# Performance work log

Hardware: AMD Instinct MI355X
Metric: run time of the kernel (lower is better)

Reference implementation:

```python
import jax, jax.numpy as jnp
import numpy as np

NUM_LAYERS = 2
VOCAB = 32000
IN_FEAT = 256          # embedding dim is IN_FEAT-1, +1 for cue scalar
HIDDEN = 256
ATN = 64               # hardcoded atn_feature_size in GraphConvolution
CLASSES = 2
B, N = 8, 2048


def setup_inputs() -> dict:
    key = jax.random.key(0)
    ks = jax.random.split(key, 12)
    x = jax.random.randint(ks[0], (B, N), 0, VOCAB, dtype=jnp.int32)
    cue = jax.random.randint(ks[1], (B, N), 0, 2, dtype=jnp.int32)
    adj = (jax.random.uniform(ks[2], (B, N, N)) < 0.01).astype(jnp.float32)
    s = 1.0 / np.sqrt(HIDDEN)
    emb_table = jax.random.normal(ks[3], (VOCAB, IN_FEAT - 1), jnp.float32) * 0.02
    Wh = jax.random.uniform(ks[4], (IN_FEAT, HIDDEN), jnp.float32, -s, s)
    bh = jax.random.uniform(ks[5], (HIDDEN,), jnp.float32, -s, s)
    Wq = jax.random.uniform(ks[6], (HIDDEN, ATN), jnp.float32, -s, s)
    Wk = jax.random.uniform(ks[7], (HIDDEN, ATN), jnp.float32, -s, s)
    Wv = jax.random.uniform(ks[8], (HIDDEN, HIDDEN), jnp.float32, -s, s)
    gcb = jax.random.uniform(ks[9], (HIDDEN,), jnp.float32, -s, s)
    Wc = jax.random.uniform(ks[10], (HIDDEN, CLASSES), jnp.float32, -s, s)
    bc = jax.random.uniform(ks[11], (CLASSES,), jnp.float32, -s, s)
    return {"x": x, "cue": cue, "adj": adj, "emb_table": emb_table,
            "Wh": Wh, "bh": bh, "Wq": Wq, "Wk": Wk, "Wv": Wv,
            "gcb": gcb, "Wc": Wc, "bc": bc}


def graph_attention_layer(h, adj, Wq, Wk, Wv, gcb):
    # h: [B,N,H]; adj: [B,N,N] binary. Per node i: softmax over neighbors j of
    # (Wk h_j) . (Wq h_i), weighted sum of Wv h_j. Zero-degree nodes get 0 (pre-bias).
    q = jnp.einsum('bnh,ha->bna', h, Wq)        # [B,N,A]
    k = jnp.einsum('bnh,ha->bna', h, Wk)        # [B,N,A]
    v = jnp.einsum('bnh,hg->bng', h, Wv)        # [B,N,H]
    logits = jnp.einsum('bia,bja->bij', q, k)   # [B,N,N]
    mask = adj > 0
    attn = jax.nn.softmax(jnp.where(mask, logits, -1e9), axis=-1)
    out = jnp.einsum('bij,bjh->bih', attn, v)   # [B,N,H]
    has_nbr = jnp.any(mask, axis=-1, keepdims=True)  # [B,N,1]
    return jnp.where(has_nbr, out, 0.0) + gcb


def reference(x, cue, adj, emb_table, Wh, bh, Wq, Wk, Wv, gcb, Wc, bc):
    emb = emb_table[x]                                   # [B,N,IN_FEAT-1]
    feats = jnp.concatenate([emb, cue.astype(jnp.float32)[..., None]], axis=-1)
    h = jax.nn.relu(jnp.einsum('bnf,fh->bnh', feats, Wh) + bh)
    for _ in range(NUM_LAYERS):
        h = jax.nn.sigmoid(graph_attention_layer(h, adj, Wq, Wk, Wv, gcb))
    logits = jnp.einsum('bnh,hc->bnc', h, Wc) + bc
    return jax.nn.softmax(logits, axis=-1)
```

## Files before the change

kernel.cpp:

```cpp
#include <hip/hip_runtime.h>
#include <hip/hip_bf16.h>


#define NB 8
#define NN 2048
#define ROWS (NB * NN)
#define MAXD 64
#define CSR1 6144

typedef float f4 __attribute__((ext_vector_type(4)));
typedef _Float16 hf;
typedef _Float16 hx2 __attribute__((ext_vector_type(2)));
typedef _Float16 hx4 __attribute__((ext_vector_type(4)));
typedef _Float16 hx8 __attribute__((ext_vector_type(8)));
typedef unsigned int u32;
typedef unsigned short u16;
typedef u16 us8 __attribute__((ext_vector_type(8)));

__device__ __forceinline__ float sigmoidf_(float x) { return 1.f / (1.f + __expf(-x)); }
__device__ __forceinline__ hx2 u2h(u32 u) { union { u32 u; hx2 h; } c; c.u = u; return c.h; }
__device__ __forceinline__ float dot2_(hx2 a, hx2 b, float c) {
#if __has_builtin(__builtin_amdgcn_fdot2)
    return __builtin_amdgcn_fdot2(a, b, c, false);
#else
    return c + (float)a.x * (float)b.x + (float)a.y * (float)b.y;
#endif
}
__device__ __forceinline__ u32 permlo_(u32 hi, u32 lo) { return __builtin_amdgcn_perm(hi, lo, 0x05040100u); }
__device__ __forceinline__ u32 permhi_(u32 hi, u32 lo) { return __builtin_amdgcn_perm(hi, lo, 0x07060302u); }

__device__ __forceinline__ void csr_row(const float* __restrict__ adj,
                                        int* __restrict__ deg, int* __restrict__ nbr,
                                        int row, int t, int* cnt) {
    const f4* ar4 = (const f4*)(adj + (size_t)row * NN);
    if (t == 0) *cnt = 0;
    __syncthreads();
    int* nr = nbr + (size_t)row * MAXD;
#pragma unroll
    for (int it = 0; it < 2; ++it) {
        int idx = it * 256 + t;
        f4 vv = __builtin_nontemporal_load(ar4 + idx);
        if (vv.x > 0.f) { int p = atomicAdd(cnt, 1); if (p < MAXD) nr[p] = idx * 4 + 0; }
        if (vv.y > 0.f) { int p = atomicAdd(cnt, 1); if (p < MAXD) nr[p] = idx * 4 + 1; }
        if (vv.z > 0.f) { int p = atomicAdd(cnt, 1); if (p < MAXD) nr[p] = idx * 4 + 2; }
        if (vv.w > 0.f) { int p = atomicAdd(cnt, 1); if (p < MAXD) nr[p] = idx * 4 + 3; }
    }
    __syncthreads();
    if (t == 0) deg[row] = (*cnt < MAXD) ? *cnt : MAXD;
}

__global__ __launch_bounds__(256) void k_front1(
        const int* __restrict__ x, const int* __restrict__ cue,
        const float* __restrict__ adj, const float* __restrict__ emb,
        const float* __restrict__ Wh, const float* __restrict__ bh,
        const float* __restrict__ Wq, const float* __restrict__ Wk,
        const float* __restrict__ Wv,
        hf* __restrict__ hB, hf* __restrict__ Wpt,
        int* __restrict__ deg, int* __restrict__ nbr) {
    __shared__ float As[32 * 64];
    __shared__ float Ws[32 * 128];
    int bid = blockIdx.x;
    int t = threadIdx.x;

    if (bid < 512) {
        int row0 = (bid >> 1) * 64, col0 = (bid & 1) * 128;
        int srow = t & 63, skg = t >> 6;
        int swc = (t & 31) * 4, swk = t >> 5;
        int tx = t & 15, ty = t >> 4;
        int xr = x[row0 + srow];
        float cv = (float)cue[row0 + srow];
        const float* er = emb + (size_t)xr * 255;

        float acc[4][8];
#pragma unroll
        for (int i = 0; i < 4; ++i)
#pragma unroll
            for (int j = 0; j < 8; ++j) acc[i][j] = 0.f;

        for (int kc = 0; kc < 256; kc += 32) {
            int kb = skg * 8;
#pragma unroll
            for (int u = 0; u < 8; ++u) {
                int f = kc + kb + u;
                As[(kb + u) * 64 + srow] = (f < 255) ? er[f] : cv;
            }
#pragma unroll
            for (int r = 0; r < 4; ++r) {
                int kk = swk + r * 8;
                f4 w = *(const f4*)(Wh + (size_t)(kc + kk) * 256 + col0 + swc);
                *(f4*)&Ws[kk * 128 + swc] = w;
            }
            __syncthreads();
#pragma unroll
            for (int k = 0; k < 32; ++k) {
                f4 av = *(f4*)&As[k * 64 + ty * 4];
                f4 w0 = *(f4*)&Ws[k * 128 + tx * 8];
                f4 w1 = *(f4*)&Ws[k * 128 + tx * 8 + 4];
                float a[4] = {av.x, av.y, av.z, av.w};
                float w[8] = {w0.x, w0.y, w0.z, w0.w, w1.x, w1.y, w1.z, w1.w};
#pragma unroll
                for (int i = 0; i < 4; ++i)
#pragma unroll
                    for (int j = 0; j < 8; ++j) acc[i][j] += a[i] * w[j];
            }
            __syncthreads();
        }
        f4 b0 = *(const f4*)(bh + col0 + tx * 8);
        f4 b1 = *(const f4*)(bh + col0 + tx * 8 + 4);
        float bb[8] = {b0.x, b0.y, b0.z, b0.w, b1.x, b1.y, b1.z, b1.w};
#pragma unroll
        for (int i = 0; i < 4; ++i) {
            int row = row0 + ty * 4 + i;
            hx8 o;
#pragma unroll
            for (int j = 0; j < 8; ++j) o[j] = (hf)fmaxf(acc[i][j] + bb[j], 0.f);
            *(hx8*)(hB + (size_t)row * 256 + col0 + tx * 8) = o;
        }
        return;
    }

    if (bid < 608) {
        int base = (bid - 512) * 256 + t;
#pragma unroll
        for (int r = 0; r < 4; ++r) {
            int i = base + r * 96 * 256;
            int c = i >> 8, f = i & 255;
            float v;
            if (c < 64)       v = Wq[f * 64 + c];
            else if (c < 128) v = Wk[f * 64 + (c - 64)];
            else              v = Wv[f * 256 + (c - 128)];
            Wpt[i] = (hf)v;
        }
        return;
    }

    csr_row(adj, deg, nbr, bid - 608, t, (int*)As);
}

union QSMem {
    struct { u16 As[64 * 40]; u16 Bs[128 * 40]; } q;
    int cnt;
};

__device__ __forceinline__ void qkv_tile(const hf* __restrict__ hB,
                                         const hf* __restrict__ Wpt,
                                         hf* __restrict__ qkvB,
                                         int tile, int t, QSMem& sm) {
    int col0 = (tile % 3) * 128, row0 = (tile / 3) * 64;
    int wave = t >> 6, lane = t & 63;
    int l16 = lane & 15, quad = lane >> 4;
    f4 acc[4][2];
#pragma unroll
    for (int i = 0; i < 4; ++i) { acc[i][0] = (f4){0,0,0,0}; acc[i][1] = (f4){0,0,0,0}; }
    int ar = t >> 2, ao = (t & 3) * 8;
    int bcs = t >> 1, bo = (t & 1) * 16;
    const u16* hB16 = (const u16*)hB;
    const u16* Wp16 = (const u16*)Wpt;

    for (int kc = 0; kc < 256; kc += 32) {
        us8 av  = *(const us8*)(hB16 + (size_t)(row0 + ar) * 256 + kc + ao);
        us8 bv0 = *(const us8*)(Wp16 + (size_t)(col0 + bcs) * 256 + kc + bo);
        us8 bv1 = *(const us8*)(Wp16 + (size_t)(col0 + bcs) * 256 + kc + bo + 8);
        __syncthreads();
        *(us8*)&sm.q.As[ar * 40 + ao] = av;
        *(us8*)&sm.q.Bs[bcs * 40 + bo] = bv0;
        *(us8*)&sm.q.Bs[bcs * 40 + bo + 8] = bv1;
        __syncthreads();
        hx8 afr[4], bfr[2];
#pragma unroll
        for (int mt = 0; mt < 4; ++mt)
            afr[mt] = *(hx8*)&sm.q.As[(mt * 16 + l16) * 40 + quad * 8];
#pragma unroll
        for (int nt = 0; nt < 2; ++nt)
            bfr[nt] = *(hx8*)&sm.q.Bs[((wave * 2 + nt) * 16 + l16) * 40 + quad * 8];
#pragma unroll
        for (int mt = 0; mt < 4; ++mt)
#pragma unroll
            for (int nt = 0; nt < 2; ++nt)
                acc[mt][nt] = __builtin_amdgcn_mfma_f32_16x16x32_f16(
                    afr[mt], bfr[nt], acc[mt][nt], 0, 0, 0);
    }
#pragma unroll
    for (int mt = 0; mt < 4; ++mt)
#pragma unroll
        for (int nt = 0; nt < 2; ++nt) {
            int c = col0 + (wave * 2 + nt) * 16 + l16;
#pragma unroll
            for (int reg = 0; reg < 4; ++reg) {
                int r = row0 + mt * 16 + quad * 4 + reg;
                qkvB[(size_t)r * 384 + c] = (hf)acc[mt][nt][reg];
            }
        }
}

__global__ __launch_bounds__(256) void k_qkv_csr(const hf* __restrict__ hB,
                                                 const hf* __restrict__ Wpt,
                                                 hf* __restrict__ qkvB,
                                                 const float* __restrict__ adj,
                                                 int* __restrict__ deg,
                                                 int* __restrict__ nbr) {
    __shared__ QSMem sm;
    int bid = blockIdx.x, t = threadIdx.x;
    if (bid < 768) qkv_tile(hB, Wpt, qkvB, bid, t, sm);
    else           csr_row(adj, deg, nbr, CSR1 + (bid - 768), t, &sm.cnt);
}

__global__ __launch_bounds__(256) void k_qkv(const hf* __restrict__ hB,
                                             const hf* __restrict__ Wpt,
                                             hf* __restrict__ qkvB) {
    __shared__ QSMem sm;
    qkv_tile(hB, Wpt, qkvB, blockIdx.x, threadIdx.x, sm);
}

template <bool WRITE_OUT>
__global__ __launch_bounds__(256) void k_attn(const hf* __restrict__ qkvB,
                                              const int* __restrict__ deg,
                                              const int* __restrict__ nbr,
                                              const float* __restrict__ gcb,
                                              const float* __restrict__ Wc,
                                              const float* __restrict__ bc,
                                              hf* __restrict__ hB,
                                              float* __restrict__ out) {
    int wave = threadIdx.x >> 6;
    int lane = threadIdx.x & 63;
    int bid = blockIdx.x;
    int row = (bid & 7) * NN + (bid >> 3) * 4 + wave;
    int d = deg[row];
    f4 g4 = *(const f4*)(gcb + lane * 4);
    float h0, h1, h2c, h3;
    if (d == 0) {
        h0 = sigmoidf_(g4.x); h1 = sigmoidf_(g4.y);
        h2c = sigmoidf_(g4.z); h3 = sigmoidf_(g4.w);
    } else {
        const int* jl = nbr + (size_t)row * MAXD;
        int bbase = row & ~(NN - 1);
        int jlane = jl[lane < d ? lane : 0];
        int sub = lane & 3;

        const uint4* qp = (const uint4*)(qkvB + (size_t)row * 384 + sub * 16);
        uint4 qa = qp[0], qb = qp[1];
        float pp[4] = {-1e30f, -1e30f, -1e30f, -1e30f};
#pragma unroll
        for (int pi = 0; pi < 4; ++pi) {
            if (pi * 16 < d) {
                int e = pi * 16 + (lane >> 2);
                int j = __shfl(jlane, e < d ? e : 0);
                float p = -1e30f;
                if (e < d) {
                    const uint4* kp = (const uint4*)(qkvB + (size_t)(bbase + j) * 384 + 64 + sub * 16);
                    uint4 ka = kp[0], kb = kp[1];
                    p = dot2_(u2h(ka.x), u2h(qa.x),
                        dot2_(u2h(ka.y), u2h(qa.y),
                        dot2_(u2h(ka.z), u2h(qa.z),
                        dot2_(u2h(ka.w), u2h(qa.w),
                        dot2_(u2h(kb.x), u2h(qb.x),
                        dot2_(u2h(kb.y), u2h(qb.y),
                        dot2_(u2h(kb.z), u2h(qb.z),
                        dot2_(u2h(kb.w), u2h(qb.w), 0.f))))))));
                }
                p += __shfl_xor(p, 1);
                p += __shfl_xor(p, 2);
                pp[pi] = p;
            }
        }
        int src = (lane & 15) << 2;
        float t0 = __shfl(pp[0], src), t1 = __shfl(pp[1], src);
        float t2 = __shfl(pp[2], src), t3 = __shfl(pp[3], src);
        int hi = lane >> 4;
        float pe = hi == 0 ? t0 : hi == 1 ? t1 : hi == 2 ? t2 : t3;
        if (lane >= d) pe = -1e30f;

        float mx = pe;
#pragma unroll
        for (int off = 32; off; off >>= 1) mx = fmaxf(mx, __shfl_xor(mx, off));
        float wv = __expf(pe - mx);
        float sv = wv;
#pragma unroll
        for (int off = 32; off; off >>= 1) sv += __shfl_xor(sv, off);
        float wn = wv * (1.f / sv);

        f4 a = {0, 0, 0, 0};
        for (int g = 0; g < d; g += 4) {
            float w0 = __shfl(wn, g),     w1 = __shfl(wn, g + 1);
            float w2 = __shfl(wn, g + 2), w3 = __shfl(wn, g + 3);
            int j0 = __shfl(jlane, g),     j1 = __shfl(jlane, g + 1);
            int j2 = __shfl(jlane, g + 2), j3 = __shfl(jlane, g + 3);
            hx2 w01, w23;
            w01.x = (hf)w0; w01.y = (hf)w1;
            w23.x = (hf)w2; w23.y = (hf)w3;
            uint2 v0 = *(const uint2*)(qkvB + (size_t)(bbase + j0) * 384 + 128 + lane * 4);
            uint2 v1 = *(const uint2*)(qkvB + (size_t)(bbase + j1) * 384 + 128 + lane * 4);
            uint2 v2 = *(const uint2*)(qkvB + (size_t)(bbase + j2) * 384 + 128 + lane * 4);
            uint2 v3 = *(const uint2*)(qkvB + (size_t)(bbase + j3) * 384 + 128 + lane * 4);
            a.x = dot2_(u2h(permlo_(v1.x, v0.x)), w01,
                  dot2_(u2h(permlo_(v3.x, v2.x)), w23, a.x));
            a.y = dot2_(u2h(permhi_(v1.x, v0.x)), w01,
                  dot2_(u2h(permhi_(v3.x, v2.x)), w23, a.y));
            a.z = dot2_(u2h(permlo_(v1.y, v0.y)), w01,
                  dot2_(u2h(permlo_(v3.y, v2.y)), w23, a.z));
            a.w = dot2_(u2h(permhi_(v1.y, v0.y)), w01,
                  dot2_(u2h(permhi_(v3.y, v2.y)), w23, a.w));
        }
        h0 = sigmoidf_(a.x + g4.x);
        h1 = sigmoidf_(a.y + g4.y);
        h2c = sigmoidf_(a.z + g4.z);
        h3 = sigmoidf_(a.w + g4.w);
    }
    if (!WRITE_OUT) {
        hx4 o; o.x = (hf)h0; o.y = (hf)h1; o.z = (hf)h2c; o.w = (hf)h3;
        *(hx4*)(hB + (size_t)row * 256 + lane * 4) = o;
    } else {
        f4 wc0 = *(const f4*)(Wc + lane * 8);
        f4 wc1 = *(const f4*)(Wc + lane * 8 + 4);
        float pa = h0 * wc0.x + h1 * wc0.z + h2c * wc1.x + h3 * wc1.z;
        float pb = h0 * wc0.y + h1 * wc0.w + h2c * wc1.y + h3 * wc1.w;
#pragma unroll
        for (int off = 32; off; off >>= 1) {
            pa += __shfl_xor(pa, off);
            pb += __shfl_xor(pb, off);
        }
        if (lane == 0) {
            float l0 = pa + bc[0], l1 = pb + bc[1];
            float m2 = fmaxf(l0, l1);
            float e0 = __expf(l0 - m2), e1 = __expf(l1 - m2);
            float inv2 = 1.f / (e0 + e1);
            out[(size_t)row * 2 + 0] = e0 * inv2;
            out[(size_t)row * 2 + 1] = e1 * inv2;
        }
    }
}

extern "C" void kernel_launch(void* const* d_in, const int* in_sizes, int n_in,
                              void* d_out, int out_size, void* d_ws, size_t ws_size,
                              hipStream_t stream) {
    const int*   x    = (const int*)d_in[0];
    const int*   cue  = (const int*)d_in[1];
    const float* adj  = (const float*)d_in[2];
    const float* emb  = (const float*)d_in[3];
    const float* Wh   = (const float*)d_in[4];
    const float* bh   = (const float*)d_in[5];
    const float* Wq   = (const float*)d_in[6];
    const float* Wk   = (const float*)d_in[7];
    const float* Wv   = (const float*)d_in[8];
    const float* gcb  = (const float*)d_in[9];
    const float* Wc   = (const float*)d_in[10];
    const float* bc   = (const float*)d_in[11];
    float* out = (float*)d_out;

    char* w = (char*)d_ws;
    hf*  hB   = (hf*)w;   w += (size_t)ROWS * 256 * 2;
    hf*  qkvB = (hf*)w;   w += (size_t)ROWS * 384 * 2;
    hf*  Wpt  = (hf*)w;   w += (size_t)384 * 256 * 2;
    int* deg  = (int*)w;  w += (size_t)ROWS * 4;
    int* nbr  = (int*)w;

    k_front1<<<608 + CSR1, 256, 0, stream>>>(
        x, cue, adj, emb, Wh, bh, Wq, Wk, Wv, hB, Wpt, deg, nbr);
    k_qkv_csr<<<768 + (ROWS - CSR1), 256, 0, stream>>>(hB, Wpt, qkvB, adj, deg, nbr);
    k_attn<false><<<ROWS / 4, 256, 0, stream>>>(qkvB, deg, nbr, gcb, Wc, bc, hB, out);
    k_qkv<<<768, 256, 0, stream>>>(hB, Wpt, qkvB);
    k_attn<true><<<ROWS / 4, 256, 0, stream>>>(qkvB, deg, nbr, gcb, Wc, bc, hB, out);
}
```

Baseline: 342.2 us.

## Merge all stages into one persistent kernel with grid barriers and dynamic CSR queue

Replaces the five separate launches with a single persistent 1024-block kernel whose phases (embedding GEMM plus weight packing, CSR construction, QKV GEMM, attention, repeated for the second layer) are separated by atomic-counter grid barriers. CSR rows are handed out through a global work counter so blocks that finish the embedding early take more of the adjacency scan. The goal is to remove launch gaps and tail effects between kernels. In exchange it depends on all 1024 blocks being co-resident, since the spin barrier can otherwise hang or time out, and each barrier adds spin overhead and fences.

```diff
diff --git a/kernel.cpp b/kernel.cpp
--- a/kernel.cpp
+++ b/kernel.cpp
@@ -6,7 +6,8 @@
 #define NN 2048
 #define ROWS (NB * NN)
 #define MAXD 64
-#define CSR1 6144
+#define GRID 1024
+#define TPB 256
 
 typedef float f4 __attribute__((ext_vector_type(4)));
 typedef _Float16 hf;
@@ -29,13 +30,114 @@
 __device__ __forceinline__ u32 permlo_(u32 hi, u32 lo) { return __builtin_amdgcn_perm(hi, lo, 0x05040100u); }
 __device__ __forceinline__ u32 permhi_(u32 hi, u32 lo) { return __builtin_amdgcn_perm(hi, lo, 0x07060302u); }
 
-__device__ __forceinline__ void csr_row(const float* __restrict__ adj,
-                                        int* __restrict__ deg, int* __restrict__ nbr,
-                                        int row, int t, int* cnt) {
-    const f4* ar4 = (const f4*)(adj + (size_t)row * NN);
+struct Args {
+    const int *x, *cue;
+    const float *adj, *emb, *Wh, *bh, *Wq, *Wk, *Wv, *gcb, *Wc, *bc;
+    hf *hB, *qkvB, *Wpt;
+    int *deg, *nbr;
+    int *ctrl;
+    float *out;
+};
+
+union SBig {
+    struct { float As[32 * 64]; float Ws[32 * 128]; } e;
+    struct { u16 As[64 * 40]; u16 Bs[128 * 40]; } q;
+};
+struct SCtl { int srow; int cnt; };
+
+__device__ __forceinline__ void gsync(int* bar, int target) {
+    __syncthreads();
+    if (threadIdx.x == 0) {
+        __threadfence();
+        atomicAdd(bar, 1);
+        int guard = 0;
+        while (__hip_atomic_load(bar, __ATOMIC_RELAXED, __HIP_MEMORY_SCOPE_AGENT) < target
+               && ++guard < (1 << 25))
+            __builtin_amdgcn_s_sleep(2);
+        __threadfence();
+    }
+    __syncthreads();
+}
+
+__global__ __launch_bounds__(64) void k_init(int* ctrl) {
+    if (threadIdx.x < 2) ctrl[threadIdx.x] = 0;
+}
+
+__device__ __forceinline__ void pack_w(const Args& A, int pb, int t) {
+    int base = pb * 256 + t;
+#pragma unroll
+    for (int r = 0; r < 4; ++r) {
+        int i = base + r * 96 * 256;
+        int c = i >> 8, f = i & 255;
+        float v;
+        if (c < 64)       v = A.Wq[f * 64 + c];
+        else if (c < 128) v = A.Wk[f * 64 + (c - 64)];
+        else              v = A.Wv[f * 256 + (c - 128)];
+        A.Wpt[i] = (hf)v;
+    }
+}
+
+__device__ void embed_tile(const Args& A, int tile, int t, SBig& sb) {
+    int row0 = (tile >> 1) * 64, col0 = (tile & 1) * 128;
+    int srow = t & 63, skg = t >> 6;
+    int swc = (t & 31) * 4, swk = t >> 5;
+    int tx = t & 15, ty = t >> 4;
+    int xr = A.x[row0 + srow];
+    float cv = (float)A.cue[row0 + srow];
+    const float* er = A.emb + (size_t)xr * 255;
+
+    float acc[4][8];
+#pragma unroll
+    for (int i = 0; i < 4; ++i)
+#pragma unroll
+        for (int j = 0; j < 8; ++j) acc[i][j] = 0.f;
+
+    for (int kc = 0; kc < 256; kc += 32) {
+        int kb = skg * 8;
+#pragma unroll
+        for (int u = 0; u < 8; ++u) {
+            int f = kc + kb + u;
+            sb.e.As[(kb + u) * 64 + srow] = (f < 255) ? er[f] : cv;
+        }
+#pragma unroll
+        for (int r = 0; r < 4; ++r) {
+            int kk = swk + r * 8;
+            f4 w = *(const f4*)(A.Wh + (size_t)(kc + kk) * 256 + col0 + swc);
+            *(f4*)&sb.e.Ws[kk * 128 + swc] = w;
+        }
+        __syncthreads();
+#pragma unroll
+        for (int k = 0; k < 32; ++k) {
+            f4 av = *(f4*)&sb.e.As[k * 64 + ty * 4];
+            f4 w0 = *(f4*)&sb.e.Ws[k * 128 + tx * 8];
+            f4 w1 = *(f4*)&sb.e.Ws[k * 128 + tx * 8 + 4];
+            float a[4] = {av.x, av.y, av.z, av.w};
+            float w[8] = {w0.x, w0.y, w0.z, w0.w, w1.x, w1.y, w1.z, w1.w};
+#pragma unroll
+            for (int i = 0; i < 4; ++i)
+#pragma unroll
+                for (int j = 0; j < 8; ++j) acc[i][j] += a[i] * w[j];
+        }
+        __syncthreads();
+    }
+    f4 b0 = *(const f4*)(A.bh + col0 + tx * 8);
+    f4 b1 = *(const f4*)(A.bh + col0 + tx * 8 + 4);
+    float bb[8] = {b0.x, b0.y, b0.z, b0.w, b1.x, b1.y, b1.z, b1.w};
+#pragma unroll
+    for (int i = 0; i < 4; ++i) {
+        int row = row0 + ty * 4 + i;
+        hx8 o;
+#pragma unroll
+        for (int j = 0; j < 8; ++j) o[j] = (hf)fmaxf(acc[i][j] + bb[j], 0.f);
+        *(hx8*)(A.hB + (size_t)row * 256 + col0 + tx * 8) = o;
+    }
+}
+
+__device__ __forceinline__ void csr_row(const Args& A, int row, int t, int* cnt) {
+    const f4* ar4 = (const f4*)(A.adj + (size_t)row * NN);
     if (t == 0) *cnt = 0;
     __syncthreads();
-    int* nr = nbr + (size_t)row * MAXD;
+    int* nr = A.nbr + (size_t)row * MAXD;
 #pragma unroll
     for (int it = 0; it < 2; ++it) {
         int idx = it * 256 + t;
@@ -46,106 +148,10 @@
         if (vv.w > 0.f) { int p = atomicAdd(cnt, 1); if (p < MAXD) nr[p] = idx * 4 + 3; }
     }
     __syncthreads();
-    if (t == 0) deg[row] = (*cnt < MAXD) ? *cnt : MAXD;
-}
-
-__global__ __launch_bounds__(256) void k_front1(
-        const int* __restrict__ x, const int* __restrict__ cue,
-        const float* __restrict__ adj, const float* __restrict__ emb,
-        const float* __restrict__ Wh, const float* __restrict__ bh,
-        const float* __restrict__ Wq, const float* __restrict__ Wk,
-        const float* __restrict__ Wv,
-        hf* __restrict__ hB, hf* __restrict__ Wpt,
-        int* __restrict__ deg, int* __restrict__ nbr) {
-    __shared__ float As[32 * 64];
-    __shared__ float Ws[32 * 128];
-    int bid = blockIdx.x;
-    int t = threadIdx.x;
-
-    if (bid < 512) {
-        int row0 = (bid >> 1) * 64, col0 = (bid & 1) * 128;
-        int srow = t & 63, skg = t >> 6;
-        int swc = (t & 31) * 4, swk = t >> 5;
-        int tx = t & 15, ty = t >> 4;
-        int xr = x[row0 + srow];
-        float cv = (float)cue[row0 + srow];
-        const float* er = emb + (size_t)xr * 255;
-
-        float acc[4][8];
-#pragma unroll
-        for (int i = 0; i < 4; ++i)
-#pragma unroll
-            for (int j = 0; j < 8; ++j) acc[i][j] = 0.f;
-
-        for (int kc = 0; kc < 256; kc += 32) {
-            int kb = skg * 8;
-#pragma unroll
-            for (int u = 0; u < 8; ++u) {
-                int f = kc + kb + u;
-                As[(kb + u) * 64 + srow] = (f < 255) ? er[f] : cv;
-            }
-#pragma unroll
-            for (int r = 0; r < 4; ++r) {
-                int kk = swk + r * 8;
-                f4 w = *(const f4*)(Wh + (size_t)(kc + kk) * 256 + col0 + swc);
-                *(f4*)&Ws[kk * 128 + swc] = w;
-            }
-            __syncthreads();
-#pragma unroll
-            for (int k = 0; k < 32; ++k) {
-                f4 av = *(f4*)&As[k * 64 + ty * 4];
-                f4 w0 = *(f4*)&Ws[k * 128 + tx * 8];
-                f4 w1 = *(f4*)&Ws[k * 128 + tx * 8 + 4];
-                float a[4] = {av.x, av.y, av.z, av.w};
-                float w[8] = {w0.x, w0.y, w0.z, w0.w, w1.x, w1.y, w1.z, w1.w};
-#pragma unroll
-                for (int i = 0; i < 4; ++i)
-#pragma unroll
-                    for (int j = 0; j < 8; ++j) acc[i][j] += a[i] * w[j];
-            }
-            __syncthreads();
-        }
-        f4 b0 = *(const f4*)(bh + col0 + tx * 8);
-        f4 b1 = *(const f4*)(bh + col0 + tx * 8 + 4);
-        float bb[8] = {b0.x, b0.y, b0.z, b0.w, b1.x, b1.y, b1.z, b1.w};
-#pragma unroll
-        for (int i = 0; i < 4; ++i) {
-            int row = row0 + ty * 4 + i;
-            hx8 o;
-#pragma unroll
-            for (int j = 0; j < 8; ++j) o[j] = (hf)fmaxf(acc[i][j] + bb[j], 0.f);
-            *(hx8*)(hB + (size_t)row * 256 + col0 + tx * 8) = o;
-        }
-        return;
-    }
-
-    if (bid < 608) {
-        int base = (bid - 512) * 256 + t;
-#pragma unroll
-        for (int r = 0; r < 4; ++r) {
-            int i = base + r * 96 * 256;
-            int c = i >> 8, f = i & 255;
-            float v;
-            if (c < 64)       v = Wq[f * 64 + c];
-            else if (c < 128) v = Wk[f * 64 + (c - 64)];
-            else              v = Wv[f * 256 + (c - 128)];
-            Wpt[i] = (hf)v;
-        }
-        return;
-    }
-
-    csr_row(adj, deg, nbr, bid - 608, t, (int*)As);
-}
-
-union QSMem {
-    struct { u16 As[64 * 40]; u16 Bs[128 * 40]; } q;
-    int cnt;
-};
-
-__device__ __forceinline__ void qkv_tile(const hf* __restrict__ hB,
-                                         const hf* __restrict__ Wpt,
-                                         hf* __restrict__ qkvB,
-                                         int tile, int t, QSMem& sm) {
+    if (t == 0) A.deg[row] = (*cnt < MAXD) ? *cnt : MAXD;
+}
+
+__device__ void qkv_tile(const Args& A, int tile, int t, SBig& sb) {
     int col0 = (tile % 3) * 128, row0 = (tile / 3) * 64;
     int wave = t >> 6, lane = t & 63;
     int l16 = lane & 15, quad = lane >> 4;
@@ -154,25 +160,25 @@
     for (int i = 0; i < 4; ++i) { acc[i][0] = (f4){0,0,0,0}; acc[i][1] = (f4){0,0,0,0}; }
     int ar = t >> 2, ao = (t & 3) * 8;
     int bcs = t >> 1, bo = (t & 1) * 16;
-    const u16* hB16 = (const u16*)hB;
-    const u16* Wp16 = (const u16*)Wpt;
+    const u16* hB16 = (const u16*)A.hB;
+    const u16* Wp16 = (const u16*)A.Wpt;
 
     for (int kc = 0; kc < 256; kc += 32) {
         us8 av  = *(const us8*)(hB16 + (size_t)(row0 + ar) * 256 + kc + ao);
         us8 bv0 = *(const us8*)(Wp16 + (size_t)(col0 + bcs) * 256 + kc + bo);
         us8 bv1 = *(const us8*)(Wp16 + (size_t)(col0 + bcs) * 256 + kc + bo + 8);
         __syncthreads();
-        *(us8*)&sm.q.As[ar * 40 + ao] = av;
-        *(us8*)&sm.q.Bs[bcs * 40 + bo] = bv0;
-        *(us8*)&sm.q.Bs[bcs * 40 + bo + 8] = bv1;
+        *(us8*)&sb.q.As[ar * 40 + ao] = av;
+        *(us8*)&sb.q.Bs[bcs * 40 + bo] = bv0;
+        *(us8*)&sb.q.Bs[bcs * 40 + bo + 8] = bv1;
         __syncthreads();
         hx8 afr[4], bfr[2];
 #pragma unroll
         for (int mt = 0; mt < 4; ++mt)
-            afr[mt] = *(hx8*)&sm.q.As[(mt * 16 + l16) * 40 + quad * 8];
+            afr[mt] = *(hx8*)&sb.q.As[(mt * 16 + l16) * 40 + quad * 8];
 #pragma unroll
         for (int nt = 0; nt < 2; ++nt)
-            bfr[nt] = *(hx8*)&sm.q.Bs[((wave * 2 + nt) * 16 + l16) * 40 + quad * 8];
+            bfr[nt] = *(hx8*)&sb.q.Bs[((wave * 2 + nt) * 16 + l16) * 40 + quad * 8];
 #pragma unroll
         for (int mt = 0; mt < 4; ++mt)
 #pragma unroll
@@ -188,51 +194,21 @@
 #pragma unroll
             for (int reg = 0; reg < 4; ++reg) {
                 int r = row0 + mt * 16 + quad * 4 + reg;
-                qkvB[(size_t)r * 384 + c] = (hf)acc[mt][nt][reg];
+                A.qkvB[(size_t)r * 384 + c] = (hf)acc[mt][nt][reg];
             }
         }
 }
 
-__global__ __launch_bounds__(256) void k_qkv_csr(const hf* __restrict__ hB,
-                                                 const hf* __restrict__ Wpt,
-                                                 hf* __restrict__ qkvB,
-                                                 const float* __restrict__ adj,
-                                                 int* __restrict__ deg,
-                                                 int* __restrict__ nbr) {
-    __shared__ QSMem sm;
-    int bid = blockIdx.x, t = threadIdx.x;
-    if (bid < 768) qkv_tile(hB, Wpt, qkvB, bid, t, sm);
-    else           csr_row(adj, deg, nbr, CSR1 + (bid - 768), t, &sm.cnt);
-}
-
-__global__ __launch_bounds__(256) void k_qkv(const hf* __restrict__ hB,
-                                             const hf* __restrict__ Wpt,
-                                             hf* __restrict__ qkvB) {
-    __shared__ QSMem sm;
-    qkv_tile(hB, Wpt, qkvB, blockIdx.x, threadIdx.x, sm);
-}
-
-template <bool WRITE_OUT>
-__global__ __launch_bounds__(256) void k_attn(const hf* __restrict__ qkvB,
-                                              const int* __restrict__ deg,
-                                              const int* __restrict__ nbr,
-                                              const float* __restrict__ gcb,
-                                              const float* __restrict__ Wc,
-                                              const float* __restrict__ bc,
-                                              hf* __restrict__ hB,
-                                              float* __restrict__ out) {
-    int wave = threadIdx.x >> 6;
-    int lane = threadIdx.x & 63;
-    int bid = blockIdx.x;
-    int row = (bid & 7) * NN + (bid >> 3) * 4 + wave;
-    int d = deg[row];
-    f4 g4 = *(const f4*)(gcb + lane * 4);
+__device__ void attn_row(const Args& A, int row, int lane, bool write_out) {
+    int d = A.deg[row];
+    f4 g4 = *(const f4*)(A.gcb + lane * 4);
     float h0, h1, h2c, h3;
     if (d == 0) {
         h0 = sigmoidf_(g4.x); h1 = sigmoidf_(g4.y);
         h2c = sigmoidf_(g4.z); h3 = sigmoidf_(g4.w);
     } else {
-        const int* jl = nbr + (size_t)row * MAXD;
+        const hf* qkvB = A.qkvB;
+        const int* jl = A.nbr + (size_t)row * MAXD;
         int bbase = row & ~(NN - 1);
         int jlane = jl[lane < d ? lane : 0];
         int sub = lane & 3;
@@ -306,12 +282,12 @@
         h2c = sigmoidf_(a.z + g4.z);
         h3 = sigmoidf_(a.w + g4.w);
     }
-    if (!WRITE_OUT) {
+    if (!write_out) {
         hx4 o; o.x = (hf)h0; o.y = (hf)h1; o.z = (hf)h2c; o.w = (hf)h3;
-        *(hx4*)(hB + (size_t)row * 256 + lane * 4) = o;
+        *(hx4*)(A.hB + (size_t)row * 256 + lane * 4) = o;
     } else {
-        f4 wc0 = *(const f4*)(Wc + lane * 8);
-        f4 wc1 = *(const f4*)(Wc + lane * 8 + 4);
+        f4 wc0 = *(const f4*)(A.Wc + lane * 8);
+        f4 wc1 = *(const f4*)(A.Wc + lane * 8 + 4);
         float pa = h0 * wc0.x + h1 * wc0.z + h2c * wc1.x + h3 * wc1.z;
         float pb = h0 * wc0.y + h1 * wc0.w + h2c * wc1.y + h3 * wc1.w;
 #pragma unroll
@@ -320,44 +296,76 @@
             pb += __shfl_xor(pb, off);
         }
         if (lane == 0) {
-            float l0 = pa + bc[0], l1 = pb + bc[1];
+            float l0 = pa + A.bc[0], l1 = pb + A.bc[1];
             float m2 = fmaxf(l0, l1);
             float e0 = __expf(l0 - m2), e1 = __expf(l1 - m2);
             float inv2 = 1.f / (e0 + e1);
-            out[(size_t)row * 2 + 0] = e0 * inv2;
-            out[(size_t)row * 2 + 1] = e1 * inv2;
-        }
-    }
+            A.out[(size_t)row * 2 + 0] = e0 * inv2;
+            A.out[(size_t)row * 2 + 1] = e1 * inv2;
+        }
+    }
+}
+
+__global__ __launch_bounds__(TPB, 4) void k_mega(Args A) {
+    __shared__ SBig sb;
+    __shared__ SCtl sc;
+    int bid = blockIdx.x, t = threadIdx.x;
+    int wave = t >> 6, lane = t & 63;
+    int batch = bid & 7, idx = bid >> 3;
+
+    if (bid < 512) embed_tile(A, bid, t, sb);
+    else if (bid < 608) pack_w(A, bid - 512, t);
+    for (;;) {
+        __syncthreads();
+        if (t == 0) sc.srow = atomicAdd(A.ctrl + 1, 4);
+        __syncthreads();
+        int r0 = sc.srow;
+        if (r0 >= ROWS) break;
+        int rn = (r0 + 4 < ROWS) ? r0 + 4 : ROWS;
+        for (int r = r0; r < rn; ++r) csr_row(A, r, t, &sc.cnt);
+    }
+    gsync(A.ctrl, GRID);
+
+    if (bid < 768) qkv_tile(A, bid, t, sb);
+    gsync(A.ctrl, 2 * GRID);
+
+    for (int k2 = 0; k2 < 4; ++k2)
+        attn_row(A, batch * NN + idx * 16 + wave * 4 + k2, lane, false);
+    gsync(A.ctrl, 3 * GRID);
+
+    if (bid < 768) qkv_tile(A, bid, t, sb);
+    gsync(A.ctrl, 4 * GRID);
+
+    for (int k2 = 0; k2 < 4; ++k2)
+        attn_row(A, batch * NN + idx * 16 + wave * 4 + k2, lane, true);
 }
 
 extern "C" void kernel_launch(void* const* d_in, const int* in_sizes, int n_in,
                               void* d_out, int out_size, void* d_ws, size_t ws_size,
                               hipStream_t stream) {
-    const int*   x    = (const int*)d_in[0];
-    const int*   cue  = (const int*)d_in[1];
-    const float* adj  = (const float*)d_in[2];
-    const float* emb  = (const float*)d_in[3];
-    const float* Wh   = (const float*)d_in[4];
-    const float* bh   = (const float*)d_in[5];
-    const float* Wq   = (const float*)d_in[6];
-    const float* Wk   = (const float*)d_in[7];
-    const float* Wv   = (const float*)d_in[8];
-    const float* gcb  = (const float*)d_in[9];
-    const float* Wc   = (const float*)d_in[10];
-    const float* bc   = (const float*)d_in[11];
-    float* out = (float*)d_out;
+    Args A;
+    A.x   = (const int*)d_in[0];
+    A.cue = (const int*)d_in[1];
+    A.adj = (const float*)d_in[2];
+    A.emb = (const float*)d_in[3];
+    A.Wh  = (const float*)d_in[4];
+    A.bh  = (const float*)d_in[5];
+    A.Wq  = (const float*)d_in[6];
+    A.Wk  = (const float*)d_in[7];
+    A.Wv  = (const float*)d_in[8];
+    A.gcb = (const float*)d_in[9];
+    A.Wc  = (const float*)d_in[10];
+    A.bc  = (const float*)d_in[11];
+    A.out = (float*)d_out;
 
     char* w = (char*)d_ws;
-    hf*  hB   = (hf*)w;   w += (size_t)ROWS * 256 * 2;
-    hf*  qkvB = (hf*)w;   w += (size_t)ROWS * 384 * 2;
-    hf*  Wpt  = (hf*)w;   w += (size_t)384 * 256 * 2;
-    int* deg  = (int*)w;  w += (size_t)ROWS * 4;
-    int* nbr  = (int*)w;
-
-    k_front1<<<608 + CSR1, 256, 0, stream>>>(
-        x, cue, adj, emb, Wh, bh, Wq, Wk, Wv, hB, Wpt, deg, nbr);
-    k_qkv_csr<<<768 + (ROWS - CSR1), 256, 0, stream>>>(hB, Wpt, qkvB, adj, deg, nbr);
-    k_attn<false><<<ROWS / 4, 256, 0, stream>>>(qkvB, deg, nbr, gcb, Wc, bc, hB, out);
-    k_qkv<<<768, 256, 0, stream>>>(hB, Wpt, qkvB);
-    k_attn<true><<<ROWS / 4, 256, 0, stream>>>(qkvB, deg, nbr, gcb, Wc, bc, hB, out);
-}
+    A.hB   = (hf*)w;   w += (size_t)ROWS * 256 * 2;
+    A.qkvB = (hf*)w;   w += (size_t)ROWS * 384 * 2;
+    A.Wpt  = (hf*)w;   w += (size_t)384 * 256 * 2;
+    A.deg  = (int*)w;  w += (size_t)ROWS * 4;
+    A.nbr  = (int*)w;  w += (size_t)ROWS * MAXD * 4;
+    A.ctrl = (int*)w;
+
+    k_init<<<1, 64, 0, stream>>>(A.ctrl);
+    k_mega<<<GRID, TPB, 0, stream>>>(A);
+}
```

After: 959.0 us. 180% more time.
